# Kernel tuning notes

Hardware: AMD Instinct MI355X
Metric: run time of the kernel (lower is better)

## Reference

```python
import jax, jax.numpy as jnp
import numpy as np

N, D, L, H = 4, 512, 2048, 8  # batch, feat_dim, seq_len, num_heads


def setup_inputs() -> dict:
    key = jax.random.key(0)
    k1, k2, k3, k4 = jax.random.split(key, 4)
    x = jax.random.normal(k1, (N, D, L), dtype=jnp.float32)
    w_qkv = jax.random.normal(k2, (3 * D, D, 1), dtype=jnp.float32) * 0.02   # 1x1 conv
    w_dw = jax.random.normal(k3, (3 * D, 1, 3), dtype=jnp.float32) * 0.02    # depthwise k=3
    w_proj = jax.random.normal(k4, (D, D, 1), dtype=jnp.float32) * 0.02      # 1x1 conv
    temperature = jnp.ones((1, H, 1, 1), dtype=jnp.float32)
    return {"x": x, "w_qkv": w_qkv, "w_dw": w_dw, "w_proj": w_proj, "temperature": temperature}


def _conv1x1(x, w):
    # x: (n, c_in, l), w: (c_out, c_in, 1)
    return jnp.einsum('oc,ncl->nol', w[:, :, 0], x)


def _l2norm(t, eps=1e-12):
    # matches F.normalize: t / max(||t||_2, eps) along last dim
    n = jnp.sqrt(jnp.sum(t * t, axis=-1, keepdims=True))
    return t / jnp.maximum(n, eps)


def reference(x, w_qkv, w_dw, w_proj, temperature):
    n, d, l = x.shape
    h = temperature.shape[1]
    dh = d // h

    qkv = _conv1x1(x, w_qkv)                               # (n, 3d, l)
    qkv = jax.lax.conv_general_dilated(
        qkv, w_dw, window_strides=(1,), padding=[(1, 1)],
        dimension_numbers=('NCH', 'OIH', 'NCH'),
        feature_group_count=3 * d)                          # depthwise conv, (n, 3d, l)

    q, k, v = jnp.split(qkv, 3, axis=1)                     # each (n, d, l)
    # (n, d, l) -> (n, h, dh, l) -> (n, h, l, dh)
    q = q.reshape(n, h, dh, l).transpose(0, 1, 3, 2)
    k = k.reshape(n, h, dh, l).transpose(0, 1, 3, 2)
    v = v.reshape(n, h, dh, l).transpose(0, 1, 3, 2)

    q = _l2norm(q)
    k = _l2norm(k)

    scores = jnp.einsum('nhqd,nhkd->nhqk', q, k) * temperature  # (n, h, l, l)
    attn = jax.nn.softmax(scores, axis=-1)
    out = jnp.einsum('nhqk,nhkd->nhqd', attn, v)                # (n, h, l, dh)
    out = out.transpose(0, 1, 3, 2).reshape(n, d, l)            # (n, d, l)
    return _conv1x1(out, w_proj)
```

## Files before the change

kernel.cpp:

```cpp
#include <hip/hip_runtime.h>
#include <hip/hip_bf16.h>
#include <cstdint>
#include <cstddef>

#define N_B 4
#define D_F 512
#define L_S 2048
#define H_N 8
#define DH  64
#define C3  (3*D_F)

typedef __attribute__((ext_vector_type(8)))  short short8;
typedef __attribute__((ext_vector_type(4)))  float f32x4;
typedef __attribute__((ext_vector_type(16))) float f32x16;

#if __has_builtin(__builtin_amdgcn_exp2f)
#define EXP2F(x) __builtin_amdgcn_exp2f(x)
#else
#define EXP2F(x) __expf((x) * 0.6931471805599453f)
#endif

__device__ __forceinline__ unsigned int pk_bf16(float a, float b) {
    __hip_bfloat162 h = __float22bfloat162_rn(float2{a, b});
    union { __hip_bfloat162 h; unsigned int u; } cv;
    cv.h = h;
    return cv.u;
}
__device__ __forceinline__ unsigned short bf16_rn(float f) {
    union { float f; unsigned int u; } c; c.f = f;
    unsigned int r = c.u + 0x7FFF + ((c.u >> 16) & 1);
    return (unsigned short)(r >> 16);
}
__device__ __forceinline__ float bf16_f(unsigned short h) {
    union { unsigned int u; float f; } c; c.u = ((unsigned int)h) << 16;
    return c.f;
}

__device__ __forceinline__ void gll16(const unsigned short* g, unsigned short* l) {
    __builtin_amdgcn_global_load_lds(
        (const __attribute__((address_space(1))) unsigned int*)g,
        (__attribute__((address_space(3))) unsigned int*)l,
        16, 0, 0);
}

__global__ __launch_bounds__(256) void cvt_split_w(const float* __restrict__ wq,
                                                   unsigned short* __restrict__ wq_hi,
                                                   unsigned short* __restrict__ wq_lo,
                                                   int n4q,
                                                   const float* __restrict__ wp,
                                                   unsigned short* __restrict__ wp_hi,
                                                   unsigned short* __restrict__ wp_lo,
                                                   int n4p) {
    int i = blockIdx.x * 256 + threadIdx.x;
    const float* src;
    unsigned short *hi, *lo;
    int idx;
    if (i < n4q) { src = wq; hi = wq_hi; lo = wq_lo; idx = i; }
    else if (i < n4q + n4p) { src = wp; hi = wp_hi; lo = wp_lo; idx = i - n4q; }
    else return;
    float4 v = ((const float4*)src)[idx];
    ushort4 h, l;
    h.x = bf16_rn(v.x); l.x = bf16_rn(v.x - bf16_f(h.x));
    h.y = bf16_rn(v.y); l.y = bf16_rn(v.y - bf16_f(h.y));
    h.z = bf16_rn(v.z); l.z = bf16_rn(v.z - bf16_f(h.z));
    h.w = bf16_rn(v.w); l.w = bf16_rn(v.w - bf16_f(h.w));
    ((ushort4*)hi)[idx] = h;
    ((ushort4*)lo)[idx] = l;
}

__global__ __launch_bounds__(256) void cvt_xT(const float* __restrict__ x,
                                              unsigned short* __restrict__ xT,
                                              int C) {
    __shared__ float tile[64][65];
    const int tid = threadIdx.x;
    const int l0  = blockIdx.x * 64;
    const int c0  = blockIdx.y * 64;
    const int n   = blockIdx.z;

    const float* xn = x + (size_t)n * C * L_S;
#pragma unroll
    for (int r = 0; r < 16; ++r) {
        int c = r * 4 + (tid >> 6);
        int l = tid & 63;
        tile[c][l] = xn[(size_t)(c0 + c) * L_S + l0 + l];
    }
    __syncthreads();

    unsigned short* xn_t = xT + (size_t)n * L_S * C;
#pragma unroll
    for (int r = 0; r < 8; ++r) {
        int l  = r * 8 + (tid >> 5);
        int cp = tid & 31;
        unsigned int pk = pk_bf16(tile[cp * 2][l], tile[cp * 2 + 1][l]);
        *(unsigned int*)&xn_t[(size_t)(l0 + l) * C + c0 + cp * 2] = pk;
    }
}

template<int SPLIT, int OUT_BF16>
__global__ __launch_bounds__(256) void gemm_mfma2(const unsigned short* __restrict__ Whi,
                                                  const unsigned short* __restrict__ Wlo,
                                                  const unsigned short* __restrict__ XThi,
                                                  const unsigned short* __restrict__ XTlo,
                                                  void* __restrict__ Y,
                                                  int O, int C) {
    __shared__ unsigned short Wt[SPLIT ? 2 : 1][4][128 * 8];
    __shared__ unsigned short Xt[SPLIT ? 2 : 1][4][128 * 8];

    const int tid  = threadIdx.x;
    const int lane = tid & 63;
    const int w    = tid >> 6;
    const int g    = lane >> 4;
    const int c    = lane & 15;
    const int wr   = (w >> 1) * 64;
    const int wc   = (w & 1) * 64;
    const int l0   = blockIdx.x * 128;
    const int o0   = blockIdx.y * 128;
    const int n    = blockIdx.z;

    const unsigned short* XTn_hi = XThi + (size_t)n * L_S * C;
    const unsigned short* XTn_lo = SPLIT ? (XTlo + (size_t)n * L_S * C) : nullptr;

    const int rhalf = (w & 1) * 64;
    const int cpA   = w >> 1;
    const int cpB   = 2 + (w >> 1);
    const size_t wrowA = (size_t)(o0 + rhalf + lane) * C;
    const size_t xrowA = (size_t)(l0 + rhalf + lane) * C;

    f32x4 acc[4][4];
#pragma unroll
    for (int mt = 0; mt < 4; ++mt)
#pragma unroll
        for (int nt = 0; nt < 4; ++nt) acc[mt][nt] = (f32x4){0.f, 0.f, 0.f, 0.f};

    for (int c0 = 0; c0 < C; c0 += 32) {
        __syncthreads();
        gll16(Whi + wrowA + c0 + cpA * 8, &Wt[0][cpA][rhalf * 8]);
        gll16(Whi + wrowA + c0 + cpB * 8, &Wt[0][cpB][rhalf * 8]);
        gll16(XTn_hi + xrowA + c0 + cpA * 8, &Xt[0][cpA][rhalf * 8]);
        gll16(XTn_hi + xrowA + c0 + cpB * 8, &Xt[0][cpB][rhalf * 8]);
        if (SPLIT) {
            gll16(Wlo + wrowA + c0 + cpA * 8, &Wt[1][cpA][rhalf * 8]);
            gll16(Wlo + wrowA + c0 + cpB * 8, &Wt[1][cpB][rhalf * 8]);
            gll16(XTn_lo + xrowA + c0 + cpA * 8, &Xt[1][cpA][rhalf * 8]);
            gll16(XTn_lo + xrowA + c0 + cpB * 8, &Xt[1][cpB][rhalf * 8]);
        }
        __syncthreads();

        short8 a0[4], b0[4];
#pragma unroll
        for (int mt = 0; mt < 4; ++mt) a0[mt] = *(short8*)&Wt[0][g][(wr + mt * 16 + c) * 8];
#pragma unroll
        for (int nt = 0; nt < 4; ++nt) b0[nt] = *(short8*)&Xt[0][g][(wc + nt * 16 + c) * 8];

        if (SPLIT) {
            short8 a1[4], b1[4];
#pragma unroll
            for (int mt = 0; mt < 4; ++mt) a1[mt] = *(short8*)&Wt[1][g][(wr + mt * 16 + c) * 8];
#pragma unroll
            for (int nt = 0; nt < 4; ++nt) b1[nt] = *(short8*)&Xt[1][g][(wc + nt * 16 + c) * 8];
#pragma unroll
            for (int mt = 0; mt < 4; ++mt)
#pragma unroll
                for (int nt = 0; nt < 4; ++nt) {
                    acc[mt][nt] = __builtin_amdgcn_mfma_f32_16x16x32_bf16(a0[mt], b0[nt], acc[mt][nt], 0, 0, 0);
                    acc[mt][nt] = __builtin_amdgcn_mfma_f32_16x16x32_bf16(a0[mt], b1[nt], acc[mt][nt], 0, 0, 0);
                    acc[mt][nt] = __builtin_amdgcn_mfma_f32_16x16x32_bf16(a1[mt], b0[nt], acc[mt][nt], 0, 0, 0);
                }
        } else {
#pragma unroll
            for (int mt = 0; mt < 4; ++mt)
#pragma unroll
                for (int nt = 0; nt < 4; ++nt)
                    acc[mt][nt] = __builtin_amdgcn_mfma_f32_16x16x32_bf16(a0[mt], b0[nt], acc[mt][nt], 0, 0, 0);
        }
    }

#pragma unroll
    for (int mt = 0; mt < 4; ++mt) {
#pragma unroll
        for (int r = 0; r < 4; ++r) {
            int oo = o0 + wr + mt * 16 + g * 4 + r;
            size_t rowbase = ((size_t)n * O + oo) * L_S;
#pragma unroll
            for (int nt = 0; nt < 4; ++nt) {
                int ll = l0 + wc + nt * 16 + c;
                if (OUT_BF16)
                    ((unsigned short*)Y)[rowbase + ll] = bf16_rn(acc[mt][nt][r]);
                else
                    ((float*)Y)[rowbase + ll] = acc[mt][nt][r];
            }
        }
    }
}

__global__ __launch_bounds__(256) void fused_qk2(const unsigned short* __restrict__ qkv_bf,
                                                 const float* __restrict__ w_dw,
                                                 const float* __restrict__ temp,
                                                 unsigned short* __restrict__ Qb,
                                                 unsigned short* __restrict__ Kb) {
    __shared__ unsigned short rows[64 * 264];
    __shared__ float wsm[192];
    const int tid = threadIdx.x;
    const int l0  = blockIdx.x * 256;
    const int gg  = blockIdx.y;
    const int n   = blockIdx.z;
    const int head = gg & 7;
    const int ch0  = (gg < 8) ? head * 64 : 512 + head * 64;

    if (tid < 192) wsm[tid] = w_dw[ch0 * 3 + tid];

    const unsigned short* base = qkv_bf + ((size_t)n * C3 + ch0) * L_S;
    for (int f = tid; f < 2048; f += 256) {
        int e = f >> 5, s = f & 31;
        *(uint4*)&rows[e * 264 + s * 8] = *(const uint4*)&base[(size_t)e * L_S + l0 + s * 8];
    }
    if (tid < 64) {
        rows[tid * 264 + 256] = (l0 > 0) ? base[(size_t)tid * L_S + l0 - 1] : (unsigned short)0;
    } else if (tid < 128) {
        int e = tid - 64;
        rows[e * 264 + 257] = (l0 + 256 < L_S) ? base[(size_t)e * L_S + l0 + 256] : (unsigned short)0;
    }
    __syncthreads();

    const int lL = tid;
    const int iL = (lL == 0)   ? 256 : lL - 1;
    const int iR = (lL == 255) ? 257 : lL + 1;
    float y[64];
    float s = 0.f;
#pragma unroll
    for (int e = 0; e < 64; ++e) {
        float a = bf16_f(rows[e * 264 + iL]);
        float b = bf16_f(rows[e * 264 + lL]);
        float d = bf16_f(rows[e * 264 + iR]);
        float v = wsm[e * 3 + 0] * a + wsm[e * 3 + 1] * b + wsm[e * 3 + 2] * d;
        y[e] = v;
        s += v * v;
    }
    float sc = 1.0f / fmaxf(sqrtf(s), 1e-12f);
    if (gg < 8) sc *= temp[head] * 1.44269504088896f;

    const int l = l0 + tid;
    unsigned short* dst = ((gg < 8) ? Qb : Kb) + (size_t)(n * H_N + head) * 8 * L_S * 8;
#pragma unroll
    for (int p = 0; p < 8; ++p) {
        uint4 pk = make_uint4(pk_bf16(y[8 * p + 0] * sc, y[8 * p + 1] * sc),
                              pk_bf16(y[8 * p + 2] * sc, y[8 * p + 3] * sc),
                              pk_bf16(y[8 * p + 4] * sc, y[8 * p + 5] * sc),
                              pk_bf16(y[8 * p + 6] * sc, y[8 * p + 7] * sc));
        *(uint4*)&dst[((size_t)p * L_S + l) * 8] = pk;
    }
}

__global__ __launch_bounds__(256) void fused_v2(const unsigned short* __restrict__ qkv_bf,
                                                const float* __restrict__ w_dw,
                                                unsigned short* __restrict__ Vb) {
    const int tid = threadIdx.x;
    const int e   = tid & 63;
    const int jp  = blockIdx.x * 4 + (tid >> 6);
    const int h   = blockIdx.y;
    const int n   = blockIdx.z;
    const int ch  = 1024 + h * 64 + e;
    const unsigned short* row = qkv_bf + ((size_t)n * C3 + ch) * L_S;
    const int k0 = jp * 8;

    uint4 mv = *(const uint4*)&row[k0];
    unsigned int lw = (jp > 0)   ? *(const unsigned int*)&row[k0 - 2] : 0u;
    unsigned int rw = (jp < 255) ? *(const unsigned int*)&row[k0 + 8] : 0u;

    float v[10];
    v[0] = bf16_f((unsigned short)(lw >> 16));
    v[1] = bf16_f((unsigned short)(mv.x & 0xFFFF));
    v[2] = bf16_f((unsigned short)(mv.x >> 16));
    v[3] = bf16_f((unsigned short)(mv.y & 0xFFFF));
    v[4] = bf16_f((unsigned short)(mv.y >> 16));
    v[5] = bf16_f((unsigned short)(mv.z & 0xFFFF));
    v[6] = bf16_f((unsigned short)(mv.z >> 16));
    v[7] = bf16_f((unsigned short)(mv.w & 0xFFFF));
    v[8] = bf16_f((unsigned short)(mv.w >> 16));
    v[9] = bf16_f((unsigned short)(rw & 0xFFFF));

    float w0 = w_dw[ch * 3 + 0], w1 = w_dw[ch * 3 + 1], w2 = w_dw[ch * 3 + 2];
    unsigned int o[4];
#pragma unroll
    for (int i = 0; i < 4; ++i) {
        float y0 = w0 * v[2 * i + 0] + w1 * v[2 * i + 1] + w2 * v[2 * i + 2];
        float y1 = w0 * v[2 * i + 1] + w1 * v[2 * i + 2] + w2 * v[2 * i + 3];
        o[i] = pk_bf16(y0, y1);
    }
    uint4 ov = make_uint4(o[0], o[1], o[2], o[3]);
    *(uint4*)&Vb[(((size_t)(n * H_N + h) * 256 + jp) * 512) + e * 8] = ov;
}

__global__ __launch_bounds__(512, 4) void attn13(const unsigned short* __restrict__ Qb,
                                                 const unsigned short* __restrict__ Kb,
                                                 const unsigned short* __restrict__ Vb,
                                                 const float* __restrict__ temp,
                                                 unsigned short* __restrict__ aoT_hi,
                                                 unsigned short* __restrict__ aoT_lo) {
    __shared__ unsigned short KV[32768];
    __shared__ float smA[128], smB[128];
    float* OtB = (float*)(KV + 16384);
    float* OtA = (float*)KV;

    const int tid  = threadIdx.x;
    const int lane = tid & 63;
    const int w    = tid >> 6;
    const int g2   = w >> 2;
    const int wv   = w & 3;
    const int c32  = lane & 31;
    const int h    = lane >> 5;
    const int q0   = blockIdx.x * 128;
    const int hd   = blockIdx.y;
    const int n    = blockIdx.z;

    const size_t hb = (size_t)(n * H_N + hd);
    const unsigned short* Qh = Qb + hb * 8 * L_S * 8;
    const unsigned short* Kh = Kb + hb * 8 * L_S * 8;
    const unsigned short* Vh = Vb + hb * 256 * 512;
    const float t2    = temp[hd] * 1.44269504088896f;
    const float negm2 = -fabsf(t2);

    unsigned short* myKV = KV + g2 * 16384;
    unsigned short* Qs   = KV + 24576;

    for (int tk = w; tk < 48; tk += 8) {
        if (tk < 16) {
            int p = tk >> 1, hh = tk & 1;
            gll16(Qh + ((size_t)p * L_S + q0 + hh * 64 + lane) * 8, Qs + p * 1024 + hh * 512);
        } else if (tk < 24) {
            int p = tk - 16;
            gll16(Kh + ((size_t)p * L_S + lane) * 8, KV + p * 512);
        } else if (tk < 32) {
            int p = tk - 24;
            gll16(Vh + ((size_t)p * 512 + lane * 8), KV + 4096 + p * 512);
        } else if (tk < 40) {
            int p = tk - 32;
            gll16(Kh + ((size_t)p * L_S + 64 + lane) * 8, KV + 16384 + p * 512);
        } else {
            int p = tk - 40;
            gll16(Vh + ((size_t)(8 + p) * 512 + lane * 8), KV + 16384 + 4096 + p * 512);
        }
    }
    __syncthreads();

    short8 qa[4];
#pragma unroll
    for (int es = 0; es < 4; ++es)
        qa[es] = *(short8*)&Qs[(es * 2 + h) * 1024 + (wv * 32 + c32) * 8];
    __syncthreads();

    f32x16 acc0, acc1;
#pragma unroll
    for (int i = 0; i < 16; ++i) { acc0[i] = 0.f; acc1[i] = 0.f; }
    float sumP = 0.f;

    for (int it = 0; it < 16; ++it) {
        const int cur = it & 1;
        const unsigned short* B = myKV + cur * 8192;

        if (it < 15) {
            const int kb = ((it + 1) * 2 + g2) * 64;
            unsigned short* D = myKV + (cur ^ 1) * 8192;
            gll16(Kh + ((size_t)wv * L_S + kb + lane) * 8,            D + wv * 512);
            gll16(Kh + ((size_t)(wv + 4) * L_S + kb + lane) * 8,      D + (wv + 4) * 512);
            gll16(Vh + ((size_t)(kb / 8 + wv) * 512 + lane * 8),      D + 4096 + wv * 512);
            gll16(Vh + ((size_t)(kb / 8 + wv + 4) * 512 + lane * 8),  D + 4096 + (wv + 4) * 512);
        }

        f32x16 sf0, sf1;
#pragma unroll
        for (int i = 0; i < 16; ++i) { sf0[i] = 0.f; sf1[i] = 0.f; }
#pragma unroll
        for (int es = 0; es < 4; ++es) {
            short8 ka0 = *(short8*)&B[(es * 2 + h) * 512 + c32 * 8];
            short8 ka1 = *(short8*)&B[(es * 2 + h) * 512 + (32 + c32) * 8];
            sf0 = __builtin_amdgcn_mfma_f32_32x32x16_bf16(ka0, qa[es], sf0, 0, 0, 0);
            sf1 = __builtin_amdgcn_mfma_f32_32x32x16_bf16(ka1, qa[es], sf1, 0, 0, 0);
        }

        short8 pa[4];
        {
            unsigned int W_[16], R_[16];
#pragma unroll
            for (int G = 0; G < 4; ++G) {
                float p0 = EXP2F(sf0[4*G+0] + negm2);
                float p1 = EXP2F(sf0[4*G+1] + negm2);
                float p2 = EXP2F(sf0[4*G+2] + negm2);
                float p3 = EXP2F(sf0[4*G+3] + negm2);
                sumP += (p0 + p1) + (p2 + p3);
                W_[2*G]   = pk_bf16(p0, p1);
                W_[2*G+1] = pk_bf16(p2, p3);
                float u0 = EXP2F(sf1[4*G+0] + negm2);
                float u1 = EXP2F(sf1[4*G+1] + negm2);
                float u2 = EXP2F(sf1[4*G+2] + negm2);
                float u3 = EXP2F(sf1[4*G+3] + negm2);
                sumP += (u0 + u1) + (u2 + u3);
                W_[8+2*G]   = pk_bf16(u0, u1);
                W_[8+2*G+1] = pk_bf16(u2, u3);
            }
#pragma unroll
            for (int j = 0; j < 16; ++j) R_[j] = __shfl_xor(W_[j], 32);
#pragma unroll
            for (int ks = 0; ks < 4; ++ks) {
                const int bb = (ks >> 1) * 8;
                const int m4 = (ks & 1) * 4;
                unsigned int a0 = h ? R_[bb+m4+2] : W_[bb+m4+0];
                unsigned int a1 = h ? R_[bb+m4+3] : W_[bb+m4+1];
                unsigned int a2 = h ? W_[bb+m4+2] : R_[bb+m4+0];
                unsigned int a3 = h ? W_[bb+m4+3] : R_[bb+m4+1];
                uint4 pu = make_uint4(a0, a1, a2, a3);
                pa[ks] = *(short8*)&pu;
            }
        }

#pragma unroll
        for (int ks = 0; ks < 4; ++ks) {
            short8 vb0 = *(short8*)&B[4096 + (ks * 2 + h) * 512 + c32 * 8];
            short8 vb1 = *(short8*)&B[4096 + (ks * 2 + h) * 512 + (32 + c32) * 8];
            acc0 = __builtin_amdgcn_mfma_f32_32x32x16_bf16(pa[ks], vb0, acc0, 0, 0, 0);
            acc1 = __builtin_amdgcn_mfma_f32_32x32x16_bf16(pa[ks], vb1, acc1, 0, 0, 0);
        }

        __syncthreads();
    }

    sumP += __shfl_xor(sumP, 32);

    if (g2 == 1) {
        smB[wv * 32 + c32] = sumP;
#pragma unroll
        for (int r = 0; r < 16; ++r) {
            int ql = (r & 3) + 8 * (r >> 2) + 4 * h;
            int qg = wv * 32 + ql;
            OtB[qg * 64 + c32]      = acc0[r];
            OtB[qg * 64 + 32 + c32] = acc1[r];
        }
    } else {
        smA[wv * 32 + c32] = sumP;
    }
    __syncthreads();

    if (g2 == 0) {
#pragma unroll
        for (int r = 0; r < 16; ++r) {
            int ql = (r & 3) + 8 * (r >> 2) + 4 * h;
            int qg = wv * 32 + ql;
            float inv = 1.0f / (smA[qg] + smB[qg]);
            float v0 = (acc0[r] + OtB[qg * 64 + c32])      * inv;
            float v1 = (acc1[r] + OtB[qg * 64 + 32 + c32]) * inv;
            OtA[qg * 64 + (c32 ^ (qg & 31))]        = v0;
            OtA[qg * 64 + ((32 + c32) ^ (qg & 31))] = v1;
        }
    }
    __syncthreads();

    for (int tt = tid; tt < 8192; tt += 512) {
        int qq = tt >> 6, e = tt & 63;
        float v = OtA[qq * 64 + (e ^ (qq & 31))];
        unsigned short hi_ = bf16_rn(v);
        unsigned short lo_ = bf16_rn(v - bf16_f(hi_));
        size_t off = ((size_t)n * L_S + q0 + qq) * D_F + hd * 64 + e;
        aoT_hi[off] = hi_;
        aoT_lo[off] = lo_;
    }
}

extern "C" void kernel_launch(void* const* d_in, const int* in_sizes, int n_in,
                              void* d_out, int out_size, void* d_ws, size_t ws_size,
                              hipStream_t stream) {
    const float* x      = (const float*)d_in[0];
    const float* w_qkv  = (const float*)d_in[1];
    const float* w_dw   = (const float*)d_in[2];
    const float* w_proj = (const float*)d_in[3];
    const float* temp   = (const float*)d_in[4];
    float* out = (float*)d_out;

    const size_t WQE = (size_t)C3 * D_F;
    const size_t WPE = (size_t)D_F * D_F;

    char* ws = (char*)d_ws;
    unsigned short* qkv_bf = (unsigned short*)ws;
    unsigned short* Qb     = (unsigned short*)(ws + 25165824);
    unsigned short* Kb     = (unsigned short*)(ws + 33554432);
    unsigned short* Vb     = (unsigned short*)(ws + 41943040);
    unsigned short* xT     = (unsigned short*)(ws + 50331648);
    unsigned short* aoT_lo = (unsigned short*)(ws + 58720256);
    unsigned short* wq_hi  = (unsigned short*)(ws + 67108864);
    unsigned short* wq_lo  = wq_hi + WQE;
    unsigned short* wp_hi  = (unsigned short*)(ws + 70254592);
    unsigned short* wp_lo  = wp_hi + WPE;
    unsigned short* aoT_hi = xT;

    cvt_xT<<<dim3(L_S / 64, D_F / 64, N_B), 256, 0, stream>>>(x, xT, D_F);
    {
        int n4q = (int)(WQE / 4), n4p = (int)(WPE / 4);
        cvt_split_w<<<dim3((n4q + n4p + 255) / 256), 256, 0, stream>>>(
            w_qkv, wq_hi, wq_lo, n4q, w_proj, wp_hi, wp_lo, n4p);
    }

    gemm_mfma2<0, 1><<<dim3(L_S / 128, C3 / 128, N_B), 256, 0, stream>>>(
        wq_hi, nullptr, xT, nullptr, qkv_bf, C3, D_F);

    fused_qk2<<<dim3(L_S / 256, 16, N_B), 256, 0, stream>>>(qkv_bf, w_dw, temp, Qb, Kb);
    fused_v2<<<dim3(64, H_N, N_B), 256, 0, stream>>>(qkv_bf, w_dw, Vb);

    attn13<<<dim3(L_S / 128, H_N, N_B), 512, 0, stream>>>(Qb, Kb, Vb, temp, aoT_hi, aoT_lo);

    gemm_mfma2<1, 0><<<dim3(L_S / 128, D_F / 128, N_B), 256, 0, stream>>>(
        wp_hi, wp_lo, aoT_hi, aoT_lo, out, D_F, D_F);
}
```

Measured before the change: 147.9 us.

## Use single fp16 projection GEMM and permlane32 swaps for P fragments

Replaces the split hi/lo bf16 three-MFMA projection GEMM with a single fp16 MFMA GEMM, so attention writes one fp16 output and the projection weights become fp16. This removes the extra lo-part loads, stores and two thirds of the projection MFMAs. Separately, the attention kernel's cross-half exchange of the packed softmax probabilities now uses permlane32_swap instead of 16 shfl_xor ops, with a runtime direction check. The trade-off is lower accuracy in the output projection (fp16 mantissa instead of about 16-bit split bf16), which could hurt tolerance.

```diff
diff --git a/kernel.cpp b/kernel.cpp
--- a/kernel.cpp
+++ b/kernel.cpp
@@ -1,5 +1,6 @@
 #include <hip/hip_runtime.h>
 #include <hip/hip_bf16.h>
+#include <hip/hip_fp16.h>
 #include <cstdint>
 #include <cstddef>
 
@@ -35,6 +36,11 @@
     union { unsigned int u; float f; } c; c.u = ((unsigned int)h) << 16;
     return c.f;
 }
+__device__ __forceinline__ unsigned short f16_bits(float f) {
+    union { __half h; unsigned short u; } c;
+    c.h = __float2half(f);
+    return c.u;
+}
 
 __device__ __forceinline__ void gll16(const unsigned short* g, unsigned short* l) {
     __builtin_amdgcn_global_load_lds(
@@ -43,29 +49,25 @@
         16, 0, 0);
 }
 
-__global__ __launch_bounds__(256) void cvt_split_w(const float* __restrict__ wq,
-                                                   unsigned short* __restrict__ wq_hi,
-                                                   unsigned short* __restrict__ wq_lo,
-                                                   int n4q,
-                                                   const float* __restrict__ wp,
-                                                   unsigned short* __restrict__ wp_hi,
-                                                   unsigned short* __restrict__ wp_lo,
-                                                   int n4p) {
+__global__ __launch_bounds__(256) void cvt_w(const float* __restrict__ wq,
+                                             unsigned short* __restrict__ wq_h,
+                                             int n4q,
+                                             const float* __restrict__ wp,
+                                             unsigned short* __restrict__ wp_h,
+                                             int n4p) {
     int i = blockIdx.x * 256 + threadIdx.x;
-    const float* src;
-    unsigned short *hi, *lo;
-    int idx;
-    if (i < n4q) { src = wq; hi = wq_hi; lo = wq_lo; idx = i; }
-    else if (i < n4q + n4p) { src = wp; hi = wp_hi; lo = wp_lo; idx = i - n4q; }
-    else return;
-    float4 v = ((const float4*)src)[idx];
-    ushort4 h, l;
-    h.x = bf16_rn(v.x); l.x = bf16_rn(v.x - bf16_f(h.x));
-    h.y = bf16_rn(v.y); l.y = bf16_rn(v.y - bf16_f(h.y));
-    h.z = bf16_rn(v.z); l.z = bf16_rn(v.z - bf16_f(h.z));
-    h.w = bf16_rn(v.w); l.w = bf16_rn(v.w - bf16_f(h.w));
-    ((ushort4*)hi)[idx] = h;
-    ((ushort4*)lo)[idx] = l;
+    if (i < n4q) {
+        float4 v = ((const float4*)wq)[i];
+        ushort4 h;
+        h.x = bf16_rn(v.x); h.y = bf16_rn(v.y); h.z = bf16_rn(v.z); h.w = bf16_rn(v.w);
+        ((ushort4*)wq_h)[i] = h;
+    } else if (i < n4q + n4p) {
+        int idx = i - n4q;
+        float4 v = ((const float4*)wp)[idx];
+        ushort4 h;
+        h.x = f16_bits(v.x); h.y = f16_bits(v.y); h.z = f16_bits(v.z); h.w = f16_bits(v.w);
+        ((ushort4*)wp_h)[idx] = h;
+    }
 }
 
 __global__ __launch_bounds__(256) void cvt_xT(const float* __restrict__ x,
@@ -96,15 +98,13 @@
     }
 }
 
-template<int SPLIT, int OUT_BF16>
-__global__ __launch_bounds__(256) void gemm_mfma2(const unsigned short* __restrict__ Whi,
-                                                  const unsigned short* __restrict__ Wlo,
-                                                  const unsigned short* __restrict__ XThi,
-                                                  const unsigned short* __restrict__ XTlo,
+template<int FP16, int OUT_BF16>
+__global__ __launch_bounds__(256) void gemm_mfma3(const unsigned short* __restrict__ Wd,
+                                                  const unsigned short* __restrict__ XT,
                                                   void* __restrict__ Y,
                                                   int O, int C) {
-    __shared__ unsigned short Wt[SPLIT ? 2 : 1][4][128 * 8];
-    __shared__ unsigned short Xt[SPLIT ? 2 : 1][4][128 * 8];
+    __shared__ unsigned short Wt[4][128 * 8];
+    __shared__ unsigned short Xt[4][128 * 8];
 
     const int tid  = threadIdx.x;
     const int lane = tid & 63;
@@ -117,8 +117,7 @@
     const int o0   = blockIdx.y * 128;
     const int n    = blockIdx.z;
 
-    const unsigned short* XTn_hi = XThi + (size_t)n * L_S * C;
-    const unsigned short* XTn_lo = SPLIT ? (XTlo + (size_t)n * L_S * C) : nullptr;
+    const unsigned short* XTn = XT + (size_t)n * L_S * C;
 
     const int rhalf = (w & 1) * 64;
     const int cpA   = w >> 1;
@@ -134,45 +133,27 @@
 
     for (int c0 = 0; c0 < C; c0 += 32) {
         __syncthreads();
-        gll16(Whi + wrowA + c0 + cpA * 8, &Wt[0][cpA][rhalf * 8]);
-        gll16(Whi + wrowA + c0 + cpB * 8, &Wt[0][cpB][rhalf * 8]);
-        gll16(XTn_hi + xrowA + c0 + cpA * 8, &Xt[0][cpA][rhalf * 8]);
-        gll16(XTn_hi + xrowA + c0 + cpB * 8, &Xt[0][cpB][rhalf * 8]);
-        if (SPLIT) {
-            gll16(Wlo + wrowA + c0 + cpA * 8, &Wt[1][cpA][rhalf * 8]);
-            gll16(Wlo + wrowA + c0 + cpB * 8, &Wt[1][cpB][rhalf * 8]);
-            gll16(XTn_lo + xrowA + c0 + cpA * 8, &Xt[1][cpA][rhalf * 8]);
-            gll16(XTn_lo + xrowA + c0 + cpB * 8, &Xt[1][cpB][rhalf * 8]);
-        }
+        gll16(Wd  + wrowA + c0 + cpA * 8, &Wt[cpA][rhalf * 8]);
+        gll16(Wd  + wrowA + c0 + cpB * 8, &Wt[cpB][rhalf * 8]);
+        gll16(XTn + xrowA + c0 + cpA * 8, &Xt[cpA][rhalf * 8]);
+        gll16(XTn + xrowA + c0 + cpB * 8, &Xt[cpB][rhalf * 8]);
         __syncthreads();
 
         short8 a0[4], b0[4];
 #pragma unroll
-        for (int mt = 0; mt < 4; ++mt) a0[mt] = *(short8*)&Wt[0][g][(wr + mt * 16 + c) * 8];
-#pragma unroll
-        for (int nt = 0; nt < 4; ++nt) b0[nt] = *(short8*)&Xt[0][g][(wc + nt * 16 + c) * 8];
-
-        if (SPLIT) {
-            short8 a1[4], b1[4];
-#pragma unroll
-            for (int mt = 0; mt < 4; ++mt) a1[mt] = *(short8*)&Wt[1][g][(wr + mt * 16 + c) * 8];
-#pragma unroll
-            for (int nt = 0; nt < 4; ++nt) b1[nt] = *(short8*)&Xt[1][g][(wc + nt * 16 + c) * 8];
-#pragma unroll
-            for (int mt = 0; mt < 4; ++mt)
-#pragma unroll
-                for (int nt = 0; nt < 4; ++nt) {
+        for (int mt = 0; mt < 4; ++mt) a0[mt] = *(short8*)&Wt[g][(wr + mt * 16 + c) * 8];
+#pragma unroll
+        for (int nt = 0; nt < 4; ++nt) b0[nt] = *(short8*)&Xt[g][(wc + nt * 16 + c) * 8];
+
+#pragma unroll
+        for (int mt = 0; mt < 4; ++mt)
+#pragma unroll
+            for (int nt = 0; nt < 4; ++nt) {
+                if (FP16)
+                    acc[mt][nt] = __builtin_amdgcn_mfma_f32_16x16x32_f16(a0[mt], b0[nt], acc[mt][nt], 0, 0, 0);
+                else
                     acc[mt][nt] = __builtin_amdgcn_mfma_f32_16x16x32_bf16(a0[mt], b0[nt], acc[mt][nt], 0, 0, 0);
-                    acc[mt][nt] = __builtin_amdgcn_mfma_f32_16x16x32_bf16(a0[mt], b1[nt], acc[mt][nt], 0, 0, 0);
-                    acc[mt][nt] = __builtin_amdgcn_mfma_f32_16x16x32_bf16(a1[mt], b0[nt], acc[mt][nt], 0, 0, 0);
-                }
-        } else {
-#pragma unroll
-            for (int mt = 0; mt < 4; ++mt)
-#pragma unroll
-                for (int nt = 0; nt < 4; ++nt)
-                    acc[mt][nt] = __builtin_amdgcn_mfma_f32_16x16x32_bf16(a0[mt], b0[nt], acc[mt][nt], 0, 0, 0);
-        }
+            }
     }
 
 #pragma unroll
@@ -291,12 +272,11 @@
     *(uint4*)&Vb[(((size_t)(n * H_N + h) * 256 + jp) * 512) + e * 8] = ov;
 }
 
-__global__ __launch_bounds__(512, 4) void attn13(const unsigned short* __restrict__ Qb,
+__global__ __launch_bounds__(512, 4) void attn14(const unsigned short* __restrict__ Qb,
                                                  const unsigned short* __restrict__ Kb,
                                                  const unsigned short* __restrict__ Vb,
                                                  const float* __restrict__ temp,
-                                                 unsigned short* __restrict__ aoT_hi,
-                                                 unsigned short* __restrict__ aoT_lo) {
+                                                 unsigned short* __restrict__ aoT) {
     __shared__ unsigned short KV[32768];
     __shared__ float smA[128], smB[128];
     float* OtB = (float*)(KV + 16384);
@@ -322,6 +302,14 @@
 
     unsigned short* myKV = KV + g2 * 16384;
     unsigned short* Qs   = KV + 24576;
+
+    bool dirA;
+    {
+        auto tp = __builtin_amdgcn_permlane32_swap((int)lane, (int)(lane + 64), false, false);
+        unsigned xv = (unsigned)tp[0];
+        bool ok = (lane < 32) ? true : (xv == (unsigned)(lane + 32));
+        dirA = (__ballot(ok) == 0xFFFFFFFFFFFFFFFFull);
+    }
 
     for (int tk = w; tk < 48; tk += 8) {
         if (tk < 16) {
@@ -380,7 +368,7 @@
 
         short8 pa[4];
         {
-            unsigned int W_[16], R_[16];
+            unsigned int W_[16];
 #pragma unroll
             for (int G = 0; G < 4; ++G) {
                 float p0 = EXP2F(sf0[4*G+0] + negm2);
@@ -399,15 +387,17 @@
                 W_[8+2*G+1] = pk_bf16(u2, u3);
             }
 #pragma unroll
-            for (int j = 0; j < 16; ++j) R_[j] = __shfl_xor(W_[j], 32);
-#pragma unroll
             for (int ks = 0; ks < 4; ++ks) {
-                const int bb = (ks >> 1) * 8;
-                const int m4 = (ks & 1) * 4;
-                unsigned int a0 = h ? R_[bb+m4+2] : W_[bb+m4+0];
-                unsigned int a1 = h ? R_[bb+m4+3] : W_[bb+m4+1];
-                unsigned int a2 = h ? W_[bb+m4+2] : R_[bb+m4+0];
-                unsigned int a3 = h ? W_[bb+m4+3] : R_[bb+m4+1];
+                unsigned w0 = dirA ? W_[4*ks]   : W_[4*ks+2];
+                unsigned w2 = dirA ? W_[4*ks+2] : W_[4*ks];
+                unsigned w1 = dirA ? W_[4*ks+1] : W_[4*ks+3];
+                unsigned w3 = dirA ? W_[4*ks+3] : W_[4*ks+1];
+                auto r02 = __builtin_amdgcn_permlane32_swap((int)w0, (int)w2, false, false);
+                auto r13 = __builtin_amdgcn_permlane32_swap((int)w1, (int)w3, false, false);
+                unsigned a0 = dirA ? (unsigned)r02[0] : (unsigned)r02[1];
+                unsigned a2 = dirA ? (unsigned)r02[1] : (unsigned)r02[0];
+                unsigned a1 = dirA ? (unsigned)r13[0] : (unsigned)r13[1];
+                unsigned a3 = dirA ? (unsigned)r13[1] : (unsigned)r13[0];
                 uint4 pu = make_uint4(a0, a1, a2, a3);
                 pa[ks] = *(short8*)&pu;
             }
@@ -457,11 +447,8 @@
     for (int tt = tid; tt < 8192; tt += 512) {
         int qq = tt >> 6, e = tt & 63;
         float v = OtA[qq * 64 + (e ^ (qq & 31))];
-        unsigned short hi_ = bf16_rn(v);
-        unsigned short lo_ = bf16_rn(v - bf16_f(hi_));
         size_t off = ((size_t)n * L_S + q0 + qq) * D_F + hd * 64 + e;
-        aoT_hi[off] = hi_;
-        aoT_lo[off] = lo_;
+        aoT[off] = f16_bits(v);
     }
 }
 
@@ -484,28 +471,25 @@
     unsigned short* Kb     = (unsigned short*)(ws + 33554432);
     unsigned short* Vb     = (unsigned short*)(ws + 41943040);
     unsigned short* xT     = (unsigned short*)(ws + 50331648);
-    unsigned short* aoT_lo = (unsigned short*)(ws + 58720256);
-    unsigned short* wq_hi  = (unsigned short*)(ws + 67108864);
-    unsigned short* wq_lo  = wq_hi + WQE;
-    unsigned short* wp_hi  = (unsigned short*)(ws + 70254592);
-    unsigned short* wp_lo  = wp_hi + WPE;
-    unsigned short* aoT_hi = xT;
+    unsigned short* wq_h   = (unsigned short*)(ws + 58720256);
+    unsigned short* wp_h   = (unsigned short*)(ws + 60293120);
+    unsigned short* aoT    = xT;
 
     cvt_xT<<<dim3(L_S / 64, D_F / 64, N_B), 256, 0, stream>>>(x, xT, D_F);
     {
         int n4q = (int)(WQE / 4), n4p = (int)(WPE / 4);
-        cvt_split_w<<<dim3((n4q + n4p + 255) / 256), 256, 0, stream>>>(
-            w_qkv, wq_hi, wq_lo, n4q, w_proj, wp_hi, wp_lo, n4p);
-    }
-
-    gemm_mfma2<0, 1><<<dim3(L_S / 128, C3 / 128, N_B), 256, 0, stream>>>(
-        wq_hi, nullptr, xT, nullptr, qkv_bf, C3, D_F);
+        cvt_w<<<dim3((n4q + n4p + 255) / 256), 256, 0, stream>>>(
+            w_qkv, wq_h, n4q, w_proj, wp_h, n4p);
+    }
+
+    gemm_mfma3<0, 1><<<dim3(L_S / 128, C3 / 128, N_B), 256, 0, stream>>>(
+        wq_h, xT, qkv_bf, C3, D_F);
 
     fused_qk2<<<dim3(L_S / 256, 16, N_B), 256, 0, stream>>>(qkv_bf, w_dw, temp, Qb, Kb);
     fused_v2<<<dim3(64, H_N, N_B), 256, 0, stream>>>(qkv_bf, w_dw, Vb);
 
-    attn13<<<dim3(L_S / 128, H_N, N_B), 512, 0, stream>>>(Qb, Kb, Vb, temp, aoT_hi, aoT_lo);
-
-    gemm_mfma2<1, 0><<<dim3(L_S / 128, D_F / 128, N_B), 256, 0, stream>>>(
-        wp_hi, wp_lo, aoT_hi, aoT_lo, out, D_F, D_F);
-}
+    attn14<<<dim3(L_S / 128, H_N, N_B), 512, 0, stream>>>(Qb, Kb, Vb, temp, aoT);
+
+    gemm_mfma3<1, 0><<<dim3(L_S / 128, D_F / 128, N_B), 256, 0, stream>>>(
+        wp_h, aoT, out, D_F, D_F);
+}
```

New measurement: 134.4 us. -9.1%, faster.
